# Optimization experiments

Hardware: AMD Instinct MI355X
Metric: run time of the kernel (lower is better)

Reference implementation:

```python
import jax, jax.numpy as jnp
import numpy as np

B, T, M, C, H = 256, 512, 16, 16, 768  # batch, time, n_media, ctrl_dim, gru hidden


def setup_inputs() -> dict:
    key = jax.random.key(0)
    ks = jax.random.split(key, 16)
    def nrm(k, shape, s=0.05):
        return jax.random.normal(k, shape, jnp.float32) * s
    A = jnp.triu(jnp.ones((M, M), jnp.float32), 1)  # strict-upper DAG prior
    return dict(
        Xm=jax.random.uniform(ks[0], (B, T, M), jnp.float32),
        Xc=jax.random.normal(ks[1], (B, T, C), jnp.float32),
        R=jax.random.randint(ks[2], (B,), 0, 2),
        A=A,
        edge_w1=nrm(ks[3], (M, 2 * M)), edge_b1=jnp.zeros((M,), jnp.float32),
        edge_w2=nrm(ks[4], (M, M)), edge_b2=jnp.zeros((M,), jnp.float32),
        node_w=nrm(ks[5], (M, 2 * M)), node_b=jnp.zeros((M,), jnp.float32),
        W_ih=nrm(ks[6], (3 * H, M + C)), W_hh=nrm(ks[7], (3 * H, H)),
        b_ih=jnp.zeros((3 * H,), jnp.float32), b_hh=jnp.zeros((3 * H,), jnp.float32),
        wraw_w=nrm(ks[8], (M, H), 0.01), wraw_b=jnp.zeros((M,), jnp.float32),
        alpha=jnp.full((M,), 0.5, jnp.float32),
        hill_a=jax.random.uniform(ks[9], (M,), jnp.float32) * 0.8 + 0.6,
        hill_g=jax.random.uniform(ks[10], (M,), jnp.float32) * 0.3 + 0.1,
        ctrl_w=nrm(ks[11], (H, C)), ctrl_b=jnp.zeros((H,), jnp.float32),
        reg_emb=nrm(ks[12], (2, H)),
        bias=jnp.zeros((1,), jnp.float32),
        h0=jnp.zeros((1, 1, H), jnp.float32),
    )


def reference(Xm, Xc, R, A, edge_w1, edge_b1, edge_w2, edge_b2, node_w, node_b,
              W_ih, W_hh, b_ih, b_hh, wraw_w, wraw_b, alpha, hill_a, hill_g,
              ctrl_w, ctrl_b, reg_emb, bias, h0):
    Bq = Xm.shape[0]
    # --- CausalEncoder, fully batched over (B, T) ---
    send = Xm @ A.T                      # [B,T,M]
    recv = Xm @ A
    He = jax.nn.relu(jnp.concatenate([send, recv], -1) @ edge_w1.T + edge_b1)
    He = jax.nn.relu(He @ edge_w2.T + edge_b2)
    Z = jax.nn.relu(jnp.concatenate([Xm, He], -1) @ node_w.T + node_b)  # [B,T,M]
    # --- adstock: linear recurrence along time via scan ---
    a = jnp.clip(alpha, 0.0, 1.0)
    xt = jnp.swapaxes(Xm, 0, 1)          # [T,B,M]
    def ad_step(prev, x):
        cur = x + a * prev
        return cur, cur
    _, rest = jax.lax.scan(ad_step, xt[0], xt[1:])
    ads = jnp.swapaxes(jnp.concatenate([xt[:1], rest], 0), 0, 1)  # [B,T,M]
    cmax = jnp.maximum(jnp.max(ads, axis=1, keepdims=True), 1e-6)
    x_n = ads / cmax
    # --- hill saturation ---
    ha = jnp.clip(hill_a, 0.1, 3.0)
    hg = jnp.clip(hill_g, 0.1, 2.0)
    num = jnp.maximum(x_n, 0.0) ** ha
    hill = num / (num + hg ** ha + 1e-8)
    # --- GRU (PyTorch gate order r,z,n) via scan ---
    gru_in = jnp.concatenate([hill + Z, Xc], -1)       # [B,T,M+C]
    git = jnp.swapaxes(gru_in, 0, 1)                   # [T,B,M+C]
    h_init = jnp.broadcast_to(h0[0, 0], (Bq, h0.shape[-1]))
    def gru_step(h, x):
        gi = x @ W_ih.T + b_ih
        gh = h @ W_hh.T + b_hh
        ir, iz, inn = jnp.split(gi, 3, axis=-1)
        hr, hz, hn = jnp.split(gh, 3, axis=-1)
        r = jax.nn.sigmoid(ir + hr)
        z = jax.nn.sigmoid(iz + hz)
        n = jnp.tanh(inn + r * hn)
        h_new = (1.0 - z) * n + z * h
        return h_new, h_new
    _, hs = jax.lax.scan(gru_step, h_init, git)
    h_seq = jnp.swapaxes(hs, 0, 1)                     # [B,T,H]
    # --- coefficients + output heads ---
    w_pos = jax.nn.softplus(h_seq @ wraw_w.T + wraw_b)  # [B,T,M]
    w0 = 0.5 * jax.lax.stop_gradient(w_pos[:, 1]) + 0.5 * w_pos[:, 0]
    w_pos = w_pos.at[:, 0].set(w0)
    contrib = hill * w_pos
    media_term = contrib.sum(-1)                        # [B,T]
    ctrl_term = jax.nn.relu(Xc @ ctrl_w.T + ctrl_b).sum(-1) * 0.3
    reg_term = reg_emb[0].sum() * 0.3                   # original indexes with zeros
    y_scaled = media_term + ctrl_term + reg_term + bias[0]
    return y_scaled, w_pos, contrib
```

## Files before the change

### kernel.cpp

```cpp
#include <hip/hip_runtime.h>

typedef __bf16 bf16;
typedef bf16 bf16x8 __attribute__((ext_vector_type(8)));
typedef bf16 bf16x4 __attribute__((ext_vector_type(4)));
typedef float f32x4 __attribute__((ext_vector_type(4)));

#define MFMA16(a,b,c) __builtin_amdgcn_mfma_f32_16x16x32_bf16((a),(b),(c),0,0,0)

#define B_N 256
#define T_N 512
#define H_N 768
#define WROW 776

__device__ float    g_ctrl[B_N * T_N];
__device__ bf16     g_hbuf[2 * B_N * H_N];
__device__ unsigned g_flag[256 * 64];
__device__ unsigned g_members[8 * 32];
__device__ unsigned g_roster[8];
__device__ unsigned g_sync;

__device__ __forceinline__ float sigmoidf_(float x){ return 1.f/(1.f+__expf(-x)); }
__device__ __forceinline__ float tanhf_(float x){
  float e = __expf(-2.f*fabsf(x));
  float t = (1.f-e)/(1.f+e);
  return copysignf(t, x);
}
__device__ __forceinline__ float softplusf_(float x){
  return x > 20.f ? x : log1pf(__expf(x));
}
__device__ __forceinline__ bf16x8 ld_bf8(const float* p){
  f32x4 a = *(const f32x4*)p;
  f32x4 b = *(const f32x4*)(p + 4);
  bf16x8 v;
  v[0]=(bf16)a[0]; v[1]=(bf16)a[1]; v[2]=(bf16)a[2]; v[3]=(bf16)a[3];
  v[4]=(bf16)b[0]; v[5]=(bf16)b[1]; v[6]=(bf16)b[2]; v[7]=(bf16)b[3];
  return v;
}

__global__ void k_zero() {
  const int tid = threadIdx.x;
  for (int i = tid; i < 256*64; i += 256) g_flag[i] = 0u;
  if (tid < 256) g_members[tid] = 0u;
  if (tid < 8)   g_roster[tid] = 0u;
  if (tid == 0)  g_sync = 0u;
}

__global__ __launch_bounds__(256) void k_encode(
    const float* __restrict__ Xm, const float* __restrict__ Xc,
    const float* __restrict__ Aw,
    const float* __restrict__ ew1, const float* __restrict__ eb1,
    const float* __restrict__ ew2, const float* __restrict__ eb2,
    const float* __restrict__ nw,  const float* __restrict__ nb,
    const float* __restrict__ cw,  const float* __restrict__ cb,
    float* __restrict__ Zout)
{
  __shared__ float sA[16][16], sE1[16][32], sE2[16][16], sNW[16][32];
  __shared__ float sEB1[16], sEB2[16], sNB[16];
  __shared__ float sCW[768][16];
  __shared__ float sCB[768];
  const int tid = threadIdx.x;
  for (int i = tid; i < 256; i += 256) sA[i>>4][i&15] = Aw[i];
  for (int i = tid; i < 512; i += 256) sE1[i>>5][i&31] = ew1[i];
  for (int i = tid; i < 256; i += 256) sE2[i>>4][i&15] = ew2[i];
  for (int i = tid; i < 512; i += 256) sNW[i>>5][i&31] = nw[i];
  if (tid < 16) { sEB1[tid]=eb1[tid]; sEB2[tid]=eb2[tid]; sNB[tid]=nb[tid]; }
  for (int i = tid; i < 768*16; i += 256) sCW[i>>4][i&15] = cw[i];
  for (int i = tid; i < 768; i += 256) sCB[i] = cb[i];
  __syncthreads();
  const int idx = blockIdx.x*256 + tid;
  const float* xmp = Xm + (size_t)idx*16;
  const float* xcp = Xc + (size_t)idx*16;
  float xm[16], xc[16];
  #pragma unroll
  for (int j=0;j<4;j++){
    *(f32x4*)&xm[j*4] = *(const f32x4*)(xmp + j*4);
    *(f32x4*)&xc[j*4] = *(const f32x4*)(xcp + j*4);
  }
  float snd[16], rcv[16];
  #pragma unroll
  for (int i=0;i<16;i++){
    float s=0.f, r=0.f;
    #pragma unroll
    for (int j=0;j<16;j++){ s += xm[j]*sA[i][j]; r += xm[j]*sA[j][i]; }
    snd[i]=s; rcv[i]=r;
  }
  float he[16];
  #pragma unroll
  for (int i=0;i<16;i++){
    float a = sEB1[i];
    #pragma unroll
    for (int k=0;k<16;k++) a += snd[k]*sE1[i][k];
    #pragma unroll
    for (int k=0;k<16;k++) a += rcv[k]*sE1[i][16+k];
    he[i] = fmaxf(a, 0.f);
  }
  float he2[16];
  #pragma unroll
  for (int i=0;i<16;i++){
    float a = sEB2[i];
    #pragma unroll
    for (int k=0;k<16;k++) a += he[k]*sE2[i][k];
    he2[i] = fmaxf(a, 0.f);
  }
  float* zp = Zout + (size_t)idx*16;
  #pragma unroll
  for (int m=0;m<16;m++){
    float a = sNB[m];
    #pragma unroll
    for (int k=0;k<16;k++) a += xm[k]*sNW[m][k];
    #pragma unroll
    for (int k=0;k<16;k++) a += he2[k]*sNW[m][16+k];
    zp[m] = fmaxf(a, 0.f);
  }
  float cs = 0.f;
  for (int i=0;i<768;i++){
    float a = sCB[i];
    #pragma unroll
    for (int k=0;k<16;k++) a += xc[k]*sCW[i][k];
    cs += fmaxf(a, 0.f);
  }
  g_ctrl[idx] = cs * 0.3f;
}

__global__ __launch_bounds__(64) void k_adstock(
    const float* __restrict__ Xm, const float* __restrict__ alpha,
    const float* __restrict__ hill_a, const float* __restrict__ hill_g,
    float* __restrict__ Zio, float* __restrict__ hill_out)
{
  const int gid = blockIdx.x*64 + threadIdx.x;
  const int b = gid >> 4, m = gid & 15;
  float a  = fminf(fmaxf(alpha[m],  0.f),  1.f);
  float ha = fminf(fmaxf(hill_a[m], 0.1f), 3.f);
  float hg = fminf(fmaxf(hill_g[m], 0.1f), 2.f);
  float gpow = __powf(hg, ha);
  const float* xp = Xm + (size_t)b*T_N*16 + m;
  float prev = 0.f, cmax = 0.f;
  for (int t=0;t<T_N;t++){ float x = xp[(size_t)t*16]; prev = x + a*prev; cmax = fmaxf(cmax, prev); }
  cmax = fmaxf(cmax, 1e-6f);
  float inv = 1.f/cmax;
  prev = 0.f;
  float* zp  = Zio      + (size_t)b*T_N*16 + m;
  float* hp  = hill_out + (size_t)b*T_N*16 + m;
  for (int t=0;t<T_N;t++){
    float x = xp[(size_t)t*16];
    prev = x + a*prev;
    float xn  = fmaxf(prev*inv, 0.f);
    float num = __powf(xn, ha);
    float h   = num / (num + gpow + 1e-8f);
    float z   = zp[(size_t)t*16];
    hp[(size_t)t*16] = h;
    zp[(size_t)t*16] = h + z;
  }
}

__device__ __forceinline__ void poll_flags(unsigned midx, unsigned val) {
  int tries = 0;
  for (;;) {
    unsigned v = __hip_atomic_load(&g_flag[midx], __ATOMIC_RELAXED, __HIP_MEMORY_SCOPE_AGENT);
    if (__ballot(v >= val) == ~0ull) break;
    if (++tries > (1<<18)) break;
    if (tries > 8) __builtin_amdgcn_s_sleep(1);
  }
  __builtin_amdgcn_fence(__ATOMIC_ACQUIRE, "workgroup");
}

__global__ __launch_bounds__(256, 1) void k_gru(
    const float* __restrict__ Xc,
    const float* __restrict__ Wih, const float* __restrict__ Whh,
    const float* __restrict__ bih, const float* __restrict__ bhh,
    const float* __restrict__ wraww, const float* __restrict__ wrawb,
    const float* __restrict__ regemb, const float* __restrict__ bias,
    const float* __restrict__ h0,
    float* __restrict__ hillZ,
    float* __restrict__ hill,
    float* __restrict__ outy)
{
  __shared__ __align__(16) bf16 sW2[32*WROW];
  __shared__ __align__(16) bf16 sH[16*768];
  __shared__ float sGH2[2][16][100];
  __shared__ float sGIN[16][32];
  __shared__ float sHm[32][24];
  __shared__ float sBih[72], sBhh[72];
  __shared__ float sWrb[16];
  __shared__ float sScal[2];
  __shared__ unsigned sGP[2];

  const int tid = threadIdx.x;
  const int wave = tid >> 6, lane = tid & 63;
  const int quad = lane >> 4, l16 = lane & 15;
  const int rg = wave & 1;
  const int kh = wave >> 1;

  if (tid == 0) {
    unsigned x;
    asm volatile("s_getreg_b32 %0, hwreg(HW_REG_XCC_ID, 0, 32)" : "=s"(x));
    x &= 7u;
    unsigned slot = __hip_atomic_fetch_add(&g_roster[x], 1u,
                        __ATOMIC_RELAXED, __HIP_MEMORY_SCOPE_AGENT);
    if (slot < 32u)
      __hip_atomic_store(&g_members[x*32u + slot], (unsigned)blockIdx.x,
                         __ATOMIC_RELAXED, __HIP_MEMORY_SCOPE_AGENT);
    sGP[0] = x; sGP[1] = slot & 31u;
    __hip_atomic_fetch_add(&g_sync, 1u, __ATOMIC_RELEASE, __HIP_MEMORY_SCOPE_AGENT);
    int tries = 0;
    while (__hip_atomic_load(&g_sync, __ATOMIC_ACQUIRE, __HIP_MEMORY_SCOPE_AGENT) < 256u) {
      if (++tries > (1<<20)) break;
      __builtin_amdgcn_s_sleep(1);
    }
  }
  __syncthreads();
  const int g = (int)sGP[0], p = (int)sGP[1];
  const int j0 = p*24;
  const int s_own = (p >= 16) ? 1 : 0;
  const int bqL = p & 15;
  const int bq = g*32 + p;
  const unsigned member = __hip_atomic_load(&g_members[g*32 + (lane & 31)],
                              __ATOMIC_RELAXED, __HIP_MEMORY_SCOPE_AGENT);
  const unsigned midx0 = member * 64u;
  const unsigned myflag = (unsigned)blockIdx.x * 64u;

  for (int c = tid; c < 32*192; c += 256) {
    int rl = c / 192, off = (c - rl*192)*4;
    int L = (rl < 16) ? (32 + rl) : (64 + rl);
    f32x4 w;
    if (L < 72)      w = *(const f32x4*)&Whh[(size_t)((L/24)*768 + j0 + (L%24))*768 + off];
    else if (L < 88) w = *(const f32x4*)&wraww[(size_t)(L-72)*768 + off];
    else             { w[0]=0.f; w[1]=0.f; w[2]=0.f; w[3]=0.f; }
    bf16x4 v; v[0]=(bf16)w[0]; v[1]=(bf16)w[1]; v[2]=(bf16)w[2]; v[3]=(bf16)w[3];
    *(bf16x4*)&sW2[rl*WROW + off] = v;
  }
  if (tid < 72) {
    int grow = (tid/24)*768 + j0 + (tid%24);
    sBih[tid] = bih[grow];
    sBhh[tid] = bhh[grow];
  }
  if (tid >= 128 && tid < 144) sWrb[tid-128] = wrawb[tid-128];
  if (wave == 0) {
    float sacc = 0.f;
    for (int k = lane; k < 768; k += 64) sacc += regemb[k];
    #pragma unroll
    for (int off = 32; off; off >>= 1) sacc += __shfl_xor(sacc, off, 64);
    if (lane == 0) { sScal[0] = 0.3f*sacc; sScal[1] = bias[0]; }
  }

  bf16x8 bw0[12], bw1[12];
  {
    const int LA = (rg ? 48 : 0) + l16;
    const int LB = (rg ? 64 : 16) + l16;
    const float* rowA = Whh + (size_t)((LA/24)*768 + j0 + (LA%24))*768;
    const float* rowB = (LB < 72)
        ? (Whh + (size_t)((LB/24)*768 + j0 + (LB%24))*768)
        : (wraww + (size_t)(LB-72)*768);
    #pragma unroll
    for (int kk = 0; kk < 12; kk++) {
      const int col = (kh*12 + kk)*32 + quad*8;
      bw0[kk] = ld_bf8(rowA + col);
      bw1[kk] = ld_bf8(rowB + col);
    }
  }
  bf16x8 wf0, wf1, wf2;
  #pragma unroll
  for (int i = 0; i < 8; i++) { wf0[i]=(bf16)0.f; wf1[i]=(bf16)0.f; wf2[i]=(bf16)0.f; }
  if (kh == 0) {
    const int base = rg ? 48 : 0;
    {
      const int L = base + l16;
      wf0 = ld_bf8(Wih + (size_t)((L/24)*768 + j0 + (L%24))*32 + quad*8);
    }
    {
      const int L = base + 16 + l16;
      if (L < 72)
        wf1 = ld_bf8(Wih + (size_t)((L/24)*768 + j0 + (L%24))*32 + quad*8);
    }
    if (rg == 0) {
      const int L = 32 + l16;
      wf2 = ld_bf8(Wih + (size_t)((L/24)*768 + j0 + (L%24))*32 + quad*8);
    }
  }

  {
    unsigned* hb = (unsigned*)g_hbuf;
    for (int e = tid; e < 384; e += 256) {
      int b = e/12, j = (e - b*12)*2;
      float f0 = h0[j0+j], f1 = h0[j0+j+1];
      sHm[b][j] = f0; sHm[b][j+1] = f1;
      union { bf16 h[2]; unsigned u; } pk;
      pk.h[0] = (bf16)f0; pk.h[1] = (bf16)f1;
      hb[((size_t)(g*32+b)*H_N + j0 + j) >> 1] = pk.u;
    }
  }
  __syncthreads();
  if (tid == 0) {
    __hip_atomic_store(&g_flag[myflag],      1u, __ATOMIC_RELAXED, __HIP_MEMORY_SCOPE_AGENT);
    __hip_atomic_store(&g_flag[myflag + 32], 1u, __ATOMIC_RELAXED, __HIP_MEMORY_SCOPE_AGENT);
  }
  const float regt = sScal[0], bias0 = sScal[1];

  float wp0_r = 0.f, hl0_r = 0.f, ct0_r = 0.f;

  bf16x8 hv[6];
  const bf16* hb_base = g_hbuf;
  const int swz = (l16 & 7) << 3;

  {
    poll_flags(midx0, 1u);
    const bf16* hsrc = hb_base + (size_t)(g*32 + l16)*H_N + quad*8;
    #pragma unroll
    for (int j = 0; j < 6; j++) {
      asm volatile("global_load_dwordx4 %0, %1, off sc0"
                   : "=v"(hv[j]) : "v"(hsrc + (wave*6 + j)*32) : "memory");
    }
  }

  f32x4 xf0, xf1;
  xf0[0]=0.f; xf0[1]=0.f; xf0[2]=0.f; xf0[3]=0.f; xf1 = xf0;
  if (kh == 0) {
    const int gb0 = g*32 + l16;
    const float* hz = hillZ + (size_t)gb0*T_N*16;
    const float* xr = Xc    + (size_t)gb0*T_N*16;
    const float* src = (quad < 2) ? (hz + quad*8) : (xr + (quad-2)*8);
    xf0 = *(const f32x4*)src;
    xf1 = *(const f32x4*)(src + 4);
  }
  float hl_pf = 0.f, ct_pf = 0.f;
  if (tid < 16) {
    hl_pf = hill[(size_t)bq*T_N*16 + tid];
    if (tid == 0) ct_pf = g_ctrl[(size_t)bq*T_N];
  }

  int par = 0;
  #pragma unroll 1
  for (int t = 0; t < T_N; t++) {
    #pragma unroll 1
    for (int s = 0; s < 2; s++) {
      asm volatile("s_waitcnt vmcnt(0)"
          : "+v"(hv[0]),"+v"(hv[1]),"+v"(hv[2]),"+v"(hv[3]),"+v"(hv[4]),"+v"(hv[5])
          :: "memory");
      {
        bf16* dst = &sH[l16*768];
        #pragma unroll
        for (int j = 0; j < 6; j++) {
          const int cv = wave*6 + j;
          *(bf16x8*)&dst[(cv*32 + quad*8) ^ swz] = hv[j];
        }
      }
      bf16x8 ax;
      if (kh == 0) {
        ax[0]=(bf16)xf0[0]; ax[1]=(bf16)xf0[1]; ax[2]=(bf16)xf0[2]; ax[3]=(bf16)xf0[3];
        ax[4]=(bf16)xf1[0]; ax[5]=(bf16)xf1[1]; ax[6]=(bf16)xf1[2]; ax[7]=(bf16)xf1[3];
      }
      __syncthreads();
      f32x4 a0; a0[0]=0.f; a0[1]=0.f; a0[2]=0.f; a0[3]=0.f;
      f32x4 a1 = a0, a2 = a0, gi0 = a0, gi1 = a0;
      if (kh == 0) {
        if (rg == 0) {
          a0 = MFMA16(ax, wf0, a0);
          a1 = MFMA16(ax, wf1, a1);
          a2 = MFMA16(ax, wf2, a2);
        } else {
          gi0 = MFMA16(ax, wf0, gi0);
          gi1 = MFMA16(ax, wf1, gi1);
        }
      }
      if (kh == 0) {
        const int sn = s ^ 1;
        int tn = (s == 1) ? t + 1 : t;
        if (tn >= T_N) tn = T_N - 1;
        const int gbn = g*32 + sn*16 + l16;
        const float* hz = hillZ + ((size_t)gbn*T_N + tn)*16;
        const float* xr = Xc    + ((size_t)gbn*T_N + tn)*16;
        const float* src = (quad < 2) ? (hz + quad*8) : (xr + (quad-2)*8);
        xf0 = *(const f32x4*)src;
        xf1 = *(const f32x4*)(src + 4);
      }
      {
        const bf16* hrow = &sH[l16*768];
        const int rl3 = (rg ? 16 : 0) + l16;
        #pragma unroll
        for (int kk = 0; kk < 12; kk++) {
          const int kt = kh*12 + kk;
          bf16x8 ha = *(const bf16x8*)&hrow[(kt*32 + quad*8) ^ swz];
          a0 = MFMA16(ha, bw0[kk], a0);
          a1 = MFMA16(ha, bw1[kk], a1);
          a2 = MFMA16(ha, *(const bf16x8*)&sW2[rl3*WROW + kt*32 + quad*8], a2);
        }
      }
      {
        const int c0 = rg*48 + l16;
        #pragma unroll
        for (int r = 0; r < 4; r++) {
          const int rb = quad*4 + r;
          sGH2[kh][rb][c0]    = a0[r];
          sGH2[kh][rb][c0+16] = a1[r];
          sGH2[kh][rb][c0+32] = a2[r];
        }
        if (kh == 0 && rg == 1) {
          #pragma unroll
          for (int r = 0; r < 4; r++) {
            const int rb = quad*4 + r;
            sGIN[rb][l16]      = gi0[r];
            sGIN[rb][16 + l16] = gi1[r];
          }
        }
      }
      __syncthreads();
      const bool own = (s_own == s);
      float hd_s = 0.f;
      if (own && tid < 16) hd_s = sGH2[0][bqL][72+tid] + sGH2[1][bqL][72+tid];
      if (!(t == T_N - 1 && s == 1)) {
        const int sn2 = s ^ 1;
        const int tn2 = s ? (t + 1) : t;
        poll_flags(midx0 + (unsigned)(sn2*32), (unsigned)(tn2 + 1));
        const bf16* hsrc2 = hb_base + (size_t)(tn2 & 1)*B_N*H_N
                          + (size_t)(g*32 + sn2*16 + l16)*H_N + quad*8;
        #pragma unroll
        for (int j = 0; j < 6; j++) {
          asm volatile("global_load_dwordx4 %0, %1, off sc0"
                       : "=v"(hv[j]) : "v"(hsrc2 + (wave*6 + j)*32) : "memory");
        }
      }
      if (tid >= 64) {
        const int e = tid - 64;
        const int b = e / 12, jp = (e - b*12)*2;
        const int bg = s*16 + b;
        unsigned* hnxt = (unsigned*)(g_hbuf + (size_t)(1-par)*B_N*H_N);
        float hn0, hn1;
        {
          const int j = jp;
          float gh_r = sGH2[0][b][j]    + sGH2[1][b][j];
          float gh_z = sGH2[0][b][24+j] + sGH2[1][b][24+j];
          float gh_n = sGH2[0][b][48+j] + sGH2[1][b][48+j];
          float rr = sigmoidf_(gh_r + sBih[j]    + sBhh[j]);
          float zz = sigmoidf_(gh_z + sBih[24+j] + sBhh[24+j]);
          float nn = tanhf_(sGIN[b][j] + sBih[48+j] + rr*(gh_n + sBhh[48+j]));
          hn0 = (1.f-zz)*nn + zz*sHm[bg][j];
        }
        {
          const int j = jp + 1;
          float gh_r = sGH2[0][b][j]    + sGH2[1][b][j];
          float gh_z = sGH2[0][b][24+j] + sGH2[1][b][24+j];
          float gh_n = sGH2[0][b][48+j] + sGH2[1][b][48+j];
          float rr = sigmoidf_(gh_r + sBih[j]    + sBhh[j]);
          float zz = sigmoidf_(gh_z + sBih[24+j] + sBhh[24+j]);
          float nn = tanhf_(sGIN[b][j] + sBih[48+j] + rr*(gh_n + sBhh[48+j]));
          hn1 = (1.f-zz)*nn + zz*sHm[bg][j];
        }
        sHm[bg][jp] = hn0; sHm[bg][jp+1] = hn1;
        union { bf16 h[2]; unsigned w; } pk;
        pk.h[0] = (bf16)hn0; pk.h[1] = (bf16)hn1;
        hnxt[((size_t)(g*32+bg)*H_N + j0 + jp) >> 1] = pk.w;
      }
      __syncthreads();
      if (tid == 0)
        __hip_atomic_store(&g_flag[myflag + s*32], (unsigned)(t + 2),
                           __ATOMIC_RELAXED, __HIP_MEMORY_SCOPE_AGENT);
      if (own) {
        if (t > 0 && tid < 16) {
          const int tt = t - 1;
          float wp = softplusf_(hd_s + sWrb[tid]);
          float hl = hl_pf;
          if (tt == 0) { wp0_r = wp; hl0_r = hl; ct0_r = ct_pf; }
          else {
            size_t o = (size_t)bq*T_N + tt;
            float cv = hl*wp;
            hillZ[o*16 + tid] = wp;
            hill[o*16 + tid]  = cv;
            float cs = cv;
            cs += __shfl_xor(cs, 8, 64);
            cs += __shfl_xor(cs, 4, 64);
            cs += __shfl_xor(cs, 2, 64);
            cs += __shfl_xor(cs, 1, 64);
            if (tid == 0) outy[o] = cs + ct_pf + regt + bias0;
            if (tt == 1) {
              float w0 = 0.5f*(wp + wp0_r);
              float c0v = hl0_r*w0;
              size_t o0 = (size_t)bq*T_N;
              hillZ[o0*16 + tid] = w0;
              hill[o0*16 + tid]  = c0v;
              float cs0 = c0v;
              cs0 += __shfl_xor(cs0, 8, 64);
              cs0 += __shfl_xor(cs0, 4, 64);
              cs0 += __shfl_xor(cs0, 2, 64);
              cs0 += __shfl_xor(cs0, 1, 64);
              if (tid == 0) outy[o0] = cs0 + ct0_r + regt + bias0;
            }
          }
        }
        if (tid < 16) {
          hl_pf = hill[((size_t)bq*T_N + t)*16 + tid];
          if (tid == 0) ct_pf = g_ctrl[(size_t)bq*T_N + t];
        }
      }
    }
    par ^= 1;
  }

  {
    const int s = s_own;
    poll_flags(midx0 + (unsigned)(s*32), (unsigned)(T_N + 1));
    const bf16* hsrc = hb_base + (size_t)par*B_N*H_N
                     + (size_t)(g*32 + s*16 + l16)*H_N + quad*8;
    bf16x8 hv2[6];
    #pragma unroll
    for (int j = 0; j < 6; j++) {
      asm volatile("global_load_dwordx4 %0, %1, off sc0"
                   : "=v"(hv2[j]) : "v"(hsrc + (wave*6 + j)*32) : "memory");
    }
    asm volatile("s_waitcnt vmcnt(0)"
        : "+v"(hv2[0]),"+v"(hv2[1]),"+v"(hv2[2]),"+v"(hv2[3]),"+v"(hv2[4]),"+v"(hv2[5])
        :: "memory");
    bf16* dst = &sH[l16*768];
    #pragma unroll
    for (int j = 0; j < 6; j++) {
      const int cv = wave*6 + j;
      *(bf16x8*)&dst[(cv*32 + quad*8) ^ swz] = hv2[j];
    }
  }
  __syncthreads();
  if (rg == 1) {
    f32x4 a1; a1[0]=0.f; a1[1]=0.f; a1[2]=0.f; a1[3]=0.f;
    f32x4 a2 = a1;
    const bf16* hrow = &sH[l16*768];
    const int rl3 = 16 + l16;
    #pragma unroll
    for (int kk = 0; kk < 12; kk++) {
      const int kt = kh*12 + kk;
      bf16x8 ha = *(const bf16x8*)&hrow[(kt*32 + quad*8) ^ swz];
      a1 = MFMA16(ha, bw1[kk], a1);
      a2 = MFMA16(ha, *(const bf16x8*)&sW2[rl3*WROW + kt*32 + quad*8], a2);
    }
    #pragma unroll
    for (int r = 0; r < 4; r++) {
      const int rb = quad*4 + r;
      sGH2[kh][rb][64 + l16] = a1[r];
      sGH2[kh][rb][80 + l16] = a2[r];
    }
  }
  __syncthreads();
  if (tid < 16) {
    const int tt = T_N - 1;
    float wp = softplusf_(sGH2[0][bqL][72+tid] + sGH2[1][bqL][72+tid] + sWrb[tid]);
    float hl = hill[((size_t)bq*T_N + tt)*16 + tid];
    size_t o = (size_t)bq*T_N + tt;
    float cv = hl*wp;
    hillZ[o*16 + tid] = wp;
    hill[o*16 + tid]  = cv;
    float cs = cv;
    cs += __shfl_xor(cs, 8, 64);
    cs += __shfl_xor(cs, 4, 64);
    cs += __shfl_xor(cs, 2, 64);
    cs += __shfl_xor(cs, 1, 64);
    if (tid == 0) outy[o] = cs + g_ctrl[o] + regt + bias0;
  }
}

extern "C" void kernel_launch(void* const* d_in, const int* in_sizes, int n_in,
                              void* d_out, int out_size, void* d_ws, size_t ws_size,
                              hipStream_t stream) {
  const float* Xm    = (const float*)d_in[0];
  const float* Xc    = (const float*)d_in[1];
  const float* Aw    = (const float*)d_in[3];
  const float* ew1   = (const float*)d_in[4];
  const float* eb1   = (const float*)d_in[5];
  const float* ew2   = (const float*)d_in[6];
  const float* eb2   = (const float*)d_in[7];
  const float* nw    = (const float*)d_in[8];
  const float* nb    = (const float*)d_in[9];
  const float* Wih   = (const float*)d_in[10];
  const float* Whh   = (const float*)d_in[11];
  const float* bih   = (const float*)d_in[12];
  const float* bhh   = (const float*)d_in[13];
  const float* wraww = (const float*)d_in[14];
  const float* wrawb = (const float*)d_in[15];
  const float* alpha = (const float*)d_in[16];
  const float* hilla = (const float*)d_in[17];
  const float* hillg = (const float*)d_in[18];
  const float* cw    = (const float*)d_in[19];
  const float* cb    = (const float*)d_in[20];
  const float* regemb= (const float*)d_in[21];
  const float* bias  = (const float*)d_in[22];
  const float* h0    = (const float*)d_in[23];

  float* outy = (float*)d_out;
  float* outw = outy + 256*512;
  float* outc = outw + 256*512*16;

  k_zero<<<1, 256, 0, stream>>>();
  k_encode<<<512, 256, 0, stream>>>(Xm, Xc, Aw, ew1, eb1, ew2, eb2, nw, nb, cw, cb,
                                    outw);
  k_adstock<<<64, 64, 0, stream>>>(Xm, alpha, hilla, hillg, outw, outc);
  k_gru<<<dim3(256), dim3(256), 0, stream>>>(
      Xc, Wih, Whh, bih, bhh, wraww, wrawb, regemb, bias, h0,
      outw, outc, outy);
}
```

Before: 3.031 ms.

## Process both batch halves concurrently with 512-thread blocks in GRU kernel

The GRU kernel previously looped over two 16-row batch halves one after the other inside each timestep, with 4 waves. It now launches 8 waves per block, with each half of the waves owning one batch half and its own shared-memory buffers, so both halves run in parallel and the per-timestep serial chain is roughly halved. Cross-block signalling changes from a single thread storing a timestep flag to each of 3 elementwise waves doing an atomic add after draining its stores, with pollers waiting on 3*(t+2). This uses more shared memory and registers per block and changes the synchronisation protocol, which adds correctness risk.

```diff
diff --git a/kernel.cpp b/kernel.cpp
--- a/kernel.cpp
+++ b/kernel.cpp
@@ -164,7 +164,7 @@
   __builtin_amdgcn_fence(__ATOMIC_ACQUIRE, "workgroup");
 }
 
-__global__ __launch_bounds__(256, 1) void k_gru(
+__global__ __launch_bounds__(512, 1) void k_gru(
     const float* __restrict__ Xc,
     const float* __restrict__ Wih, const float* __restrict__ Whh,
     const float* __restrict__ bih, const float* __restrict__ bhh,
@@ -176,9 +176,9 @@
     float* __restrict__ outy)
 {
   __shared__ __align__(16) bf16 sW2[32*WROW];
-  __shared__ __align__(16) bf16 sH[16*768];
-  __shared__ float sGH2[2][16][100];
-  __shared__ float sGIN[16][32];
+  __shared__ __align__(16) bf16 sH[2][16*768];
+  __shared__ float sGH2[2][2][16][100];
+  __shared__ float sGIN[2][16][32];
   __shared__ float sHm[32][24];
   __shared__ float sBih[72], sBhh[72];
   __shared__ float sWrb[16];
@@ -188,8 +188,10 @@
   const int tid = threadIdx.x;
   const int wave = tid >> 6, lane = tid & 63;
   const int quad = lane >> 4, l16 = lane & 15;
-  const int rg = wave & 1;
-  const int kh = wave >> 1;
+  const int sq = wave >> 2;
+  const int wv = wave & 3;
+  const int rg = wv & 1;
+  const int kh = wv >> 1;
 
   if (tid == 0) {
     unsigned x;
@@ -219,7 +221,7 @@
   const unsigned midx0 = member * 64u;
   const unsigned myflag = (unsigned)blockIdx.x * 64u;
 
-  for (int c = tid; c < 32*192; c += 256) {
+  for (int c = tid; c < 32*192; c += 512) {
     int rl = c / 192, off = (c - rl*192)*4;
     int L = (rl < 16) ? (32 + rl) : (64 + rl);
     f32x4 w;
@@ -280,7 +282,7 @@
 
   {
     unsigned* hb = (unsigned*)g_hbuf;
-    for (int e = tid; e < 384; e += 256) {
+    for (int e = tid; e < 384; e += 512) {
       int b = e/12, j = (e - b*12)*2;
       float f0 = h0[j0+j], f1 = h0[j0+j+1];
       sHm[b][j] = f0; sHm[b][j+1] = f1;
@@ -291,8 +293,8 @@
   }
   __syncthreads();
   if (tid == 0) {
-    __hip_atomic_store(&g_flag[myflag],      1u, __ATOMIC_RELAXED, __HIP_MEMORY_SCOPE_AGENT);
-    __hip_atomic_store(&g_flag[myflag + 32], 1u, __ATOMIC_RELAXED, __HIP_MEMORY_SCOPE_AGENT);
+    __hip_atomic_store(&g_flag[myflag],      3u, __ATOMIC_RELAXED, __HIP_MEMORY_SCOPE_AGENT);
+    __hip_atomic_store(&g_flag[myflag + 32], 3u, __ATOMIC_RELAXED, __HIP_MEMORY_SCOPE_AGENT);
   }
   const float regt = sScal[0], bias0 = sScal[1];
 
@@ -303,19 +305,19 @@
   const int swz = (l16 & 7) << 3;
 
   {
-    poll_flags(midx0, 1u);
-    const bf16* hsrc = hb_base + (size_t)(g*32 + l16)*H_N + quad*8;
+    poll_flags(midx0 + (unsigned)(sq*32), 3u);
+    const bf16* hsrc = hb_base + (size_t)(g*32 + sq*16 + l16)*H_N + quad*8;
     #pragma unroll
     for (int j = 0; j < 6; j++) {
       asm volatile("global_load_dwordx4 %0, %1, off sc0"
-                   : "=v"(hv[j]) : "v"(hsrc + (wave*6 + j)*32) : "memory");
+                   : "=v"(hv[j]) : "v"(hsrc + (wv*6 + j)*32) : "memory");
     }
   }
 
   f32x4 xf0, xf1;
   xf0[0]=0.f; xf0[1]=0.f; xf0[2]=0.f; xf0[3]=0.f; xf1 = xf0;
   if (kh == 0) {
-    const int gb0 = g*32 + l16;
+    const int gb0 = g*32 + sq*16 + l16;
     const float* hz = hillZ + (size_t)gb0*T_N*16;
     const float* xr = Xc    + (size_t)gb0*T_N*16;
     const float* src = (quad < 2) ? (hz + quad*8) : (xr + (quad-2)*8);
@@ -328,199 +330,189 @@
     if (tid == 0) ct_pf = g_ctrl[(size_t)bq*T_N];
   }
 
-  int par = 0;
   #pragma unroll 1
   for (int t = 0; t < T_N; t++) {
-    #pragma unroll 1
-    for (int s = 0; s < 2; s++) {
-      asm volatile("s_waitcnt vmcnt(0)"
-          : "+v"(hv[0]),"+v"(hv[1]),"+v"(hv[2]),"+v"(hv[3]),"+v"(hv[4]),"+v"(hv[5])
-          :: "memory");
-      {
-        bf16* dst = &sH[l16*768];
-        #pragma unroll
-        for (int j = 0; j < 6; j++) {
-          const int cv = wave*6 + j;
-          *(bf16x8*)&dst[(cv*32 + quad*8) ^ swz] = hv[j];
-        }
-      }
-      bf16x8 ax;
-      if (kh == 0) {
-        ax[0]=(bf16)xf0[0]; ax[1]=(bf16)xf0[1]; ax[2]=(bf16)xf0[2]; ax[3]=(bf16)xf0[3];
-        ax[4]=(bf16)xf1[0]; ax[5]=(bf16)xf1[1]; ax[6]=(bf16)xf1[2]; ax[7]=(bf16)xf1[3];
-      }
-      __syncthreads();
-      f32x4 a0; a0[0]=0.f; a0[1]=0.f; a0[2]=0.f; a0[3]=0.f;
-      f32x4 a1 = a0, a2 = a0, gi0 = a0, gi1 = a0;
-      if (kh == 0) {
-        if (rg == 0) {
-          a0 = MFMA16(ax, wf0, a0);
-          a1 = MFMA16(ax, wf1, a1);
-          a2 = MFMA16(ax, wf2, a2);
-        } else {
-          gi0 = MFMA16(ax, wf0, gi0);
-          gi1 = MFMA16(ax, wf1, gi1);
-        }
-      }
-      if (kh == 0) {
-        const int sn = s ^ 1;
-        int tn = (s == 1) ? t + 1 : t;
-        if (tn >= T_N) tn = T_N - 1;
-        const int gbn = g*32 + sn*16 + l16;
-        const float* hz = hillZ + ((size_t)gbn*T_N + tn)*16;
-        const float* xr = Xc    + ((size_t)gbn*T_N + tn)*16;
-        const float* src = (quad < 2) ? (hz + quad*8) : (xr + (quad-2)*8);
-        xf0 = *(const f32x4*)src;
-        xf1 = *(const f32x4*)(src + 4);
-      }
-      {
-        const bf16* hrow = &sH[l16*768];
-        const int rl3 = (rg ? 16 : 0) + l16;
-        #pragma unroll
-        for (int kk = 0; kk < 12; kk++) {
-          const int kt = kh*12 + kk;
-          bf16x8 ha = *(const bf16x8*)&hrow[(kt*32 + quad*8) ^ swz];
-          a0 = MFMA16(ha, bw0[kk], a0);
-          a1 = MFMA16(ha, bw1[kk], a1);
-          a2 = MFMA16(ha, *(const bf16x8*)&sW2[rl3*WROW + kt*32 + quad*8], a2);
-        }
-      }
-      {
-        const int c0 = rg*48 + l16;
+    asm volatile("s_waitcnt vmcnt(0)"
+        : "+v"(hv[0]),"+v"(hv[1]),"+v"(hv[2]),"+v"(hv[3]),"+v"(hv[4]),"+v"(hv[5])
+        :: "memory");
+    {
+      bf16* dst = &sH[sq][l16*768];
+      #pragma unroll
+      for (int j = 0; j < 6; j++) {
+        const int cv = wv*6 + j;
+        *(bf16x8*)&dst[(cv*32 + quad*8) ^ swz] = hv[j];
+      }
+    }
+    bf16x8 ax;
+    if (kh == 0) {
+      ax[0]=(bf16)xf0[0]; ax[1]=(bf16)xf0[1]; ax[2]=(bf16)xf0[2]; ax[3]=(bf16)xf0[3];
+      ax[4]=(bf16)xf1[0]; ax[5]=(bf16)xf1[1]; ax[6]=(bf16)xf1[2]; ax[7]=(bf16)xf1[3];
+    }
+    __syncthreads();
+    f32x4 a0; a0[0]=0.f; a0[1]=0.f; a0[2]=0.f; a0[3]=0.f;
+    f32x4 a1 = a0, a2 = a0, gi0 = a0, gi1 = a0;
+    if (kh == 0) {
+      if (rg == 0) {
+        a0 = MFMA16(ax, wf0, a0);
+        a1 = MFMA16(ax, wf1, a1);
+        a2 = MFMA16(ax, wf2, a2);
+      } else {
+        gi0 = MFMA16(ax, wf0, gi0);
+        gi1 = MFMA16(ax, wf1, gi1);
+      }
+    }
+    if (kh == 0) {
+      int tn = t + 1; if (tn >= T_N) tn = T_N - 1;
+      const int gbn = g*32 + sq*16 + l16;
+      const float* hz = hillZ + ((size_t)gbn*T_N + tn)*16;
+      const float* xr = Xc    + ((size_t)gbn*T_N + tn)*16;
+      const float* src = (quad < 2) ? (hz + quad*8) : (xr + (quad-2)*8);
+      xf0 = *(const f32x4*)src;
+      xf1 = *(const f32x4*)(src + 4);
+    }
+    {
+      const bf16* hrow = &sH[sq][l16*768];
+      const int rl3 = (rg ? 16 : 0) + l16;
+      #pragma unroll
+      for (int kk = 0; kk < 12; kk++) {
+        const int kt = kh*12 + kk;
+        bf16x8 ha = *(const bf16x8*)&hrow[(kt*32 + quad*8) ^ swz];
+        a0 = MFMA16(ha, bw0[kk], a0);
+        a1 = MFMA16(ha, bw1[kk], a1);
+        a2 = MFMA16(ha, *(const bf16x8*)&sW2[rl3*WROW + kt*32 + quad*8], a2);
+      }
+    }
+    {
+      const int c0 = rg*48 + l16;
+      #pragma unroll
+      for (int r = 0; r < 4; r++) {
+        const int rb = quad*4 + r;
+        sGH2[sq][kh][rb][c0]    = a0[r];
+        sGH2[sq][kh][rb][c0+16] = a1[r];
+        sGH2[sq][kh][rb][c0+32] = a2[r];
+      }
+      if (kh == 0 && rg == 1) {
         #pragma unroll
         for (int r = 0; r < 4; r++) {
           const int rb = quad*4 + r;
-          sGH2[kh][rb][c0]    = a0[r];
-          sGH2[kh][rb][c0+16] = a1[r];
-          sGH2[kh][rb][c0+32] = a2[r];
+          sGIN[sq][rb][l16]      = gi0[r];
+          sGIN[sq][rb][16 + l16] = gi1[r];
         }
-        if (kh == 0 && rg == 1) {
-          #pragma unroll
-          for (int r = 0; r < 4; r++) {
-            const int rb = quad*4 + r;
-            sGIN[rb][l16]      = gi0[r];
-            sGIN[rb][16 + l16] = gi1[r];
+      }
+    }
+    __syncthreads();
+    float hd_s = 0.f;
+    if (tid < 16) hd_s = sGH2[s_own][0][bqL][72+tid] + sGH2[s_own][1][bqL][72+tid];
+    if (wv != 0) {
+      const int e = (wv - 1)*64 + lane;
+      const int b = e / 12, jp = (e - b*12)*2;
+      const int bg = sq*16 + b;
+      unsigned* hnxt = (unsigned*)(g_hbuf + (size_t)((t+1)&1)*B_N*H_N);
+      float hn0, hn1;
+      {
+        const int j = jp;
+        float gh_r = sGH2[sq][0][b][j]    + sGH2[sq][1][b][j];
+        float gh_z = sGH2[sq][0][b][24+j] + sGH2[sq][1][b][24+j];
+        float gh_n = sGH2[sq][0][b][48+j] + sGH2[sq][1][b][48+j];
+        float rr = sigmoidf_(gh_r + sBih[j]    + sBhh[j]);
+        float zz = sigmoidf_(gh_z + sBih[24+j] + sBhh[24+j]);
+        float nn = tanhf_(sGIN[sq][b][j] + sBih[48+j] + rr*(gh_n + sBhh[48+j]));
+        hn0 = (1.f-zz)*nn + zz*sHm[bg][j];
+      }
+      {
+        const int j = jp + 1;
+        float gh_r = sGH2[sq][0][b][j]    + sGH2[sq][1][b][j];
+        float gh_z = sGH2[sq][0][b][24+j] + sGH2[sq][1][b][24+j];
+        float gh_n = sGH2[sq][0][b][48+j] + sGH2[sq][1][b][48+j];
+        float rr = sigmoidf_(gh_r + sBih[j]    + sBhh[j]);
+        float zz = sigmoidf_(gh_z + sBih[24+j] + sBhh[24+j]);
+        float nn = tanhf_(sGIN[sq][b][j] + sBih[48+j] + rr*(gh_n + sBhh[48+j]));
+        hn1 = (1.f-zz)*nn + zz*sHm[bg][j];
+      }
+      sHm[bg][jp] = hn0; sHm[bg][jp+1] = hn1;
+      union { bf16 h[2]; unsigned w; } pk;
+      pk.h[0] = (bf16)hn0; pk.h[1] = (bf16)hn1;
+      hnxt[((size_t)(g*32+bg)*H_N + j0 + jp) >> 1] = pk.w;
+      asm volatile("s_waitcnt vmcnt(0)" ::: "memory");
+      if (lane == 0)
+        __hip_atomic_fetch_add(&g_flag[myflag + sq*32], 1u,
+                               __ATOMIC_RELAXED, __HIP_MEMORY_SCOPE_AGENT);
+    }
+    __syncthreads();
+    if (t < T_N - 1) {
+      poll_flags(midx0 + (unsigned)(sq*32), 3u*(unsigned)(t + 2));
+      const bf16* hsrc2 = hb_base + (size_t)((t+1)&1)*B_N*H_N
+                        + (size_t)(g*32 + sq*16 + l16)*H_N + quad*8;
+      #pragma unroll
+      for (int j = 0; j < 6; j++) {
+        asm volatile("global_load_dwordx4 %0, %1, off sc0"
+                     : "=v"(hv[j]) : "v"(hsrc2 + (wv*6 + j)*32) : "memory");
+      }
+    }
+    if (tid < 16) {
+      if (t > 0) {
+        const int tt = t - 1;
+        float wp = softplusf_(hd_s + sWrb[tid]);
+        float hl = hl_pf;
+        if (tt == 0) { wp0_r = wp; hl0_r = hl; ct0_r = ct_pf; }
+        else {
+          size_t o = (size_t)bq*T_N + tt;
+          float cv = hl*wp;
+          hillZ[o*16 + tid] = wp;
+          hill[o*16 + tid]  = cv;
+          float cs = cv;
+          cs += __shfl_xor(cs, 8, 64);
+          cs += __shfl_xor(cs, 4, 64);
+          cs += __shfl_xor(cs, 2, 64);
+          cs += __shfl_xor(cs, 1, 64);
+          if (tid == 0) outy[o] = cs + ct_pf + regt + bias0;
+          if (tt == 1) {
+            float w0 = 0.5f*(wp + wp0_r);
+            float c0v = hl0_r*w0;
+            size_t o0 = (size_t)bq*T_N;
+            hillZ[o0*16 + tid] = w0;
+            hill[o0*16 + tid]  = c0v;
+            float cs0 = c0v;
+            cs0 += __shfl_xor(cs0, 8, 64);
+            cs0 += __shfl_xor(cs0, 4, 64);
+            cs0 += __shfl_xor(cs0, 2, 64);
+            cs0 += __shfl_xor(cs0, 1, 64);
+            if (tid == 0) outy[o0] = cs0 + ct0_r + regt + bias0;
           }
         }
       }
-      __syncthreads();
-      const bool own = (s_own == s);
-      float hd_s = 0.f;
-      if (own && tid < 16) hd_s = sGH2[0][bqL][72+tid] + sGH2[1][bqL][72+tid];
-      if (!(t == T_N - 1 && s == 1)) {
-        const int sn2 = s ^ 1;
-        const int tn2 = s ? (t + 1) : t;
-        poll_flags(midx0 + (unsigned)(sn2*32), (unsigned)(tn2 + 1));
-        const bf16* hsrc2 = hb_base + (size_t)(tn2 & 1)*B_N*H_N
-                          + (size_t)(g*32 + sn2*16 + l16)*H_N + quad*8;
-        #pragma unroll
-        for (int j = 0; j < 6; j++) {
-          asm volatile("global_load_dwordx4 %0, %1, off sc0"
-                       : "=v"(hv[j]) : "v"(hsrc2 + (wave*6 + j)*32) : "memory");
-        }
-      }
-      if (tid >= 64) {
-        const int e = tid - 64;
-        const int b = e / 12, jp = (e - b*12)*2;
-        const int bg = s*16 + b;
-        unsigned* hnxt = (unsigned*)(g_hbuf + (size_t)(1-par)*B_N*H_N);
-        float hn0, hn1;
-        {
-          const int j = jp;
-          float gh_r = sGH2[0][b][j]    + sGH2[1][b][j];
-          float gh_z = sGH2[0][b][24+j] + sGH2[1][b][24+j];
-          float gh_n = sGH2[0][b][48+j] + sGH2[1][b][48+j];
-          float rr = sigmoidf_(gh_r + sBih[j]    + sBhh[j]);
-          float zz = sigmoidf_(gh_z + sBih[24+j] + sBhh[24+j]);
-          float nn = tanhf_(sGIN[b][j] + sBih[48+j] + rr*(gh_n + sBhh[48+j]));
-          hn0 = (1.f-zz)*nn + zz*sHm[bg][j];
-        }
-        {
-          const int j = jp + 1;
-          float gh_r = sGH2[0][b][j]    + sGH2[1][b][j];
-          float gh_z = sGH2[0][b][24+j] + sGH2[1][b][24+j];
-          float gh_n = sGH2[0][b][48+j] + sGH2[1][b][48+j];
-          float rr = sigmoidf_(gh_r + sBih[j]    + sBhh[j]);
-          float zz = sigmoidf_(gh_z + sBih[24+j] + sBhh[24+j]);
-          float nn = tanhf_(sGIN[b][j] + sBih[48+j] + rr*(gh_n + sBhh[48+j]));
-          hn1 = (1.f-zz)*nn + zz*sHm[bg][j];
-        }
-        sHm[bg][jp] = hn0; sHm[bg][jp+1] = hn1;
-        union { bf16 h[2]; unsigned w; } pk;
-        pk.h[0] = (bf16)hn0; pk.h[1] = (bf16)hn1;
-        hnxt[((size_t)(g*32+bg)*H_N + j0 + jp) >> 1] = pk.w;
-      }
-      __syncthreads();
-      if (tid == 0)
-        __hip_atomic_store(&g_flag[myflag + s*32], (unsigned)(t + 2),
-                           __ATOMIC_RELAXED, __HIP_MEMORY_SCOPE_AGENT);
-      if (own) {
-        if (t > 0 && tid < 16) {
-          const int tt = t - 1;
-          float wp = softplusf_(hd_s + sWrb[tid]);
-          float hl = hl_pf;
-          if (tt == 0) { wp0_r = wp; hl0_r = hl; ct0_r = ct_pf; }
-          else {
-            size_t o = (size_t)bq*T_N + tt;
-            float cv = hl*wp;
-            hillZ[o*16 + tid] = wp;
-            hill[o*16 + tid]  = cv;
-            float cs = cv;
-            cs += __shfl_xor(cs, 8, 64);
-            cs += __shfl_xor(cs, 4, 64);
-            cs += __shfl_xor(cs, 2, 64);
-            cs += __shfl_xor(cs, 1, 64);
-            if (tid == 0) outy[o] = cs + ct_pf + regt + bias0;
-            if (tt == 1) {
-              float w0 = 0.5f*(wp + wp0_r);
-              float c0v = hl0_r*w0;
-              size_t o0 = (size_t)bq*T_N;
-              hillZ[o0*16 + tid] = w0;
-              hill[o0*16 + tid]  = c0v;
-              float cs0 = c0v;
-              cs0 += __shfl_xor(cs0, 8, 64);
-              cs0 += __shfl_xor(cs0, 4, 64);
-              cs0 += __shfl_xor(cs0, 2, 64);
-              cs0 += __shfl_xor(cs0, 1, 64);
-              if (tid == 0) outy[o0] = cs0 + ct0_r + regt + bias0;
-            }
-          }
-        }
-        if (tid < 16) {
-          hl_pf = hill[((size_t)bq*T_N + t)*16 + tid];
-          if (tid == 0) ct_pf = g_ctrl[(size_t)bq*T_N + t];
-        }
-      }
-    }
-    par ^= 1;
+      hl_pf = hill[((size_t)bq*T_N + t)*16 + tid];
+      if (tid == 0) ct_pf = g_ctrl[(size_t)bq*T_N + t];
+    }
   }
 
   {
-    const int s = s_own;
-    poll_flags(midx0 + (unsigned)(s*32), (unsigned)(T_N + 1));
-    const bf16* hsrc = hb_base + (size_t)par*B_N*H_N
-                     + (size_t)(g*32 + s*16 + l16)*H_N + quad*8;
-    bf16x8 hv2[6];
-    #pragma unroll
-    for (int j = 0; j < 6; j++) {
-      asm volatile("global_load_dwordx4 %0, %1, off sc0"
-                   : "=v"(hv2[j]) : "v"(hsrc + (wave*6 + j)*32) : "memory");
-    }
-    asm volatile("s_waitcnt vmcnt(0)"
-        : "+v"(hv2[0]),"+v"(hv2[1]),"+v"(hv2[2]),"+v"(hv2[3]),"+v"(hv2[4]),"+v"(hv2[5])
-        :: "memory");
-    bf16* dst = &sH[l16*768];
-    #pragma unroll
-    for (int j = 0; j < 6; j++) {
-      const int cv = wave*6 + j;
-      *(bf16x8*)&dst[(cv*32 + quad*8) ^ swz] = hv2[j];
+    poll_flags(midx0 + (unsigned)(s_own*32), 3u*(unsigned)(T_N + 1));
+    if (sq == s_own) {
+      const bf16* hsrc = hb_base + (size_t)(T_N & 1)*B_N*H_N
+                       + (size_t)(g*32 + s_own*16 + l16)*H_N + quad*8;
+      bf16x8 hv2[6];
+      #pragma unroll
+      for (int j = 0; j < 6; j++) {
+        asm volatile("global_load_dwordx4 %0, %1, off sc0"
+                     : "=v"(hv2[j]) : "v"(hsrc + (wv*6 + j)*32) : "memory");
+      }
+      asm volatile("s_waitcnt vmcnt(0)"
+          : "+v"(hv2[0]),"+v"(hv2[1]),"+v"(hv2[2]),"+v"(hv2[3]),"+v"(hv2[4]),"+v"(hv2[5])
+          :: "memory");
+      bf16* dst = &sH[s_own][l16*768];
+      #pragma unroll
+      for (int j = 0; j < 6; j++) {
+        const int cv = wv*6 + j;
+        *(bf16x8*)&dst[(cv*32 + quad*8) ^ swz] = hv2[j];
+      }
     }
   }
   __syncthreads();
-  if (rg == 1) {
+  if (sq == s_own && rg == 1) {
     f32x4 a1; a1[0]=0.f; a1[1]=0.f; a1[2]=0.f; a1[3]=0.f;
     f32x4 a2 = a1;
-    const bf16* hrow = &sH[l16*768];
+    const bf16* hrow = &sH[s_own][l16*768];
     const int rl3 = 16 + l16;
     #pragma unroll
     for (int kk = 0; kk < 12; kk++) {
@@ -532,14 +524,15 @@
     #pragma unroll
     for (int r = 0; r < 4; r++) {
       const int rb = quad*4 + r;
-      sGH2[kh][rb][64 + l16] = a1[r];
-      sGH2[kh][rb][80 + l16] = a2[r];
+      sGH2[s_own][kh][rb][64 + l16] = a1[r];
+      sGH2[s_own][kh][rb][80 + l16] = a2[r];
     }
   }
   __syncthreads();
   if (tid < 16) {
     const int tt = T_N - 1;
-    float wp = softplusf_(sGH2[0][bqL][72+tid] + sGH2[1][bqL][72+tid] + sWrb[tid]);
+    float wp = softplusf_(sGH2[s_own][0][bqL][72+tid] + sGH2[s_own][1][bqL][72+tid]
+                          + sWrb[tid]);
     float hl = hill[((size_t)bq*T_N + tt)*16 + tid];
     size_t o = (size_t)bq*T_N + tt;
     float cv = hl*wp;
@@ -589,7 +582,7 @@
   k_encode<<<512, 256, 0, stream>>>(Xm, Xc, Aw, ew1, eb1, ew2, eb2, nw, nb, cw, cb,
                                     outw);
   k_adstock<<<64, 64, 0, stream>>>(Xm, alpha, hilla, hillg, outw, outc);
-  k_gru<<<dim3(256), dim3(256), 0, stream>>>(
+  k_gru<<<dim3(256), dim3(512), 0, stream>>>(
       Xc, Wih, Whh, bih, bhh, wraww, wrawb, regemb, bias, h0,
       outw, outc, outy);
 }
```

Result: faster. 2.970 ms (-2.0%).
